# Kernel tuning notes

Measured on AMD Instinct MI355X. Metric: run time of the kernel, lower is better.

The kernel has to match this reference:

```python
import jax, jax.numpy as jnp
import numpy as np
from jax import lax

EPS = 1e-5

def gelu(x):
    return jax.nn.gelu(x, approximate=False)  # torch nn.GELU default (erf)

def conv1d(x, w, b):
    # x: (N, Cin, L), w: (Cout, Cin, K), SAME padding, stride 1
    y = lax.conv_general_dilated(x, w, window_strides=(1,), padding='SAME',
                                 dimension_numbers=('NCH', 'OIH', 'NCH'))
    return y + b[None, :, None]

def setup_inputs() -> dict:
    key = jax.random.key(0)
    ks = jax.random.split(key, 16)
    B, C, P, L, D = 8, 129, 62, 20, 256
    s = lambda k, shape, fan: jax.random.normal(k, shape, jnp.float32) * (1.0 / np.sqrt(fan))
    return {
        'x': jax.random.normal(ks[0], (B, C, P, L), jnp.float32),
        'conv1_w': s(ks[1], (64, 1, 3), 3),   'conv1_b': jnp.zeros((64,), jnp.float32),
        'conv2_w': s(ks[2], (128, 64, 3), 192), 'conv2_b': jnp.zeros((128,), jnp.float32),
        'conv3_w': s(ks[3], (D, 128, 3), 384),  'conv3_b': jnp.zeros((D,), jnp.float32),
        'mix_w': s(ks[4], (C, C), C), 'mix_b': jnp.zeros((C,), jnp.float32),
        'ln_w': jnp.ones((C,), jnp.float32), 'ln_b': jnp.zeros((C,), jnp.float32),
        'proj_w': s(ks[5], (D, D), D), 'proj_b': jnp.zeros((D,), jnp.float32),
    }

def reference(x, conv1_w, conv1_b, conv2_w, conv2_b, conv3_w, conv3_b,
              mix_w, mix_b, ln_w, ln_b, proj_w, proj_b):
    B, C, P, L = x.shape
    D = conv3_w.shape[0]
    # temporal conv stack over flattened (B*C*P, 1, L)
    h = x.reshape(B * C * P, 1, L)
    h = gelu(conv1d(h, conv1_w, conv1_b))
    h = gelu(conv1d(h, conv2_w, conv2_b))
    N, Ch, Lh = h.shape
    h = h.reshape(N, Ch, Lh // 2, 2).max(axis=-1)  # MaxPool1d(2)
    h = gelu(conv1d(h, conv3_w, conv3_b))
    feat = h.mean(axis=-1)                                  # (B*C*P, D)
    feat = feat.reshape(B, C, P, D).transpose(0, 2, 1, 3)   # (B, P, C, D)
    t = feat.reshape(B * P, C, D).transpose(0, 2, 1)        # (B*P, D, C) == per-feature slices
    # channel_mix: Linear(C,C) + GELU + LayerNorm(C), vectorized over the dim axis
    m = gelu(jnp.einsum('ndc,oc->ndo', t, mix_w) + mix_b)
    mu = m.mean(axis=-1, keepdims=True)
    var = ((m - mu) ** 2).mean(axis=-1, keepdims=True)
    m = (m - mu) * lax.rsqrt(var + EPS) * ln_w + ln_b
    mixed = m.transpose(0, 2, 1).reshape(B, P, C, D)
    out = jnp.einsum('bpcd,ed->bpce', mixed, proj_w) + proj_b
    return out.transpose(0, 2, 1, 3)                        # (B, C, P, D)
```

## Files before the change

### kernel.cpp

```cpp
#include <hip/hip_runtime.h>

#define B_ 8
#define C_ 129
#define P_ 62
#define L_ 20
#define D_ 256
#define NSEG (B_*C_*P_)
#define N2   (B_*P_)
#define SEGB 8
#define NWG  (NSEG/SEGB)

#define S1 1416
#define S2 1544

#define FT_STRIDE 168
#define MT_STRIDE 264

typedef short short8 __attribute__((ext_vector_type(8)));
typedef float f32x4  __attribute__((ext_vector_type(4)));

__device__ __forceinline__ float gelu_f(float x) {
    float u   = 0.70710678f * x;
    float au  = __builtin_fabsf(u);
    float den = fmaf(0.47047f, au, 1.0f);
    float t   = __builtin_amdgcn_rcpf(den);
    float q   = fmaf(0.7478556f, t, -0.0958798f);
    q = fmaf(q, t, 0.3480242f);
    float P  = q * t;
    float z  = (-1.4426950409f * au) * au;
    float e  = __builtin_amdgcn_exp2f(z);
    float ea = fmaf(-P, e, 1.0f);
    float er = copysignf(ea, x);
    float hx = 0.5f * x;
    return fmaf(hx, er, hx);
}
__device__ __forceinline__ unsigned short f2bf(float f) {
    unsigned u = __float_as_uint(f);
    u = u + 0x7FFFu + ((u >> 16) & 1u);
    return (unsigned short)(u >> 16);
}
__device__ __forceinline__ unsigned cvt_pk_bf16(float lo, float hi) {
    unsigned r;
    asm("v_cvt_pk_bf16_f32 %0, %1, %2" : "=v"(r) : "v"(lo), "v"(hi));
    return r;
}

__global__ void prep_kernel(const float* __restrict__ w2, const float* __restrict__ w3,
                            const float* __restrict__ mw, const float* __restrict__ pw,
                            const float* __restrict__ mixb, const float* __restrict__ lnw,
                            const float* __restrict__ lnb,
                            unsigned short* __restrict__ A2p, unsigned short* __restrict__ A3p,
                            unsigned short* __restrict__ mixA, unsigned short* __restrict__ projA,
                            float* __restrict__ bmixp, float* __restrict__ lnwp,
                            float* __restrict__ lnbp) {
    int idx = blockIdx.x * blockDim.x + threadIdx.x;
    int stride = gridDim.x * blockDim.x;
    for (int f = idx; f < 6*8*64*8; f += stride) {
        int j = f & 7, ln = (f >> 3) & 63, mt = (f >> 9) & 7, kt = f >> 12;
        int co = mt*16 + (ln & 15);
        int k  = kt >> 1;
        int ci = (kt & 1)*32 + (ln >> 4)*8 + j;
        A2p[f] = f2bf(w2[(co*64 + ci)*3 + k]);
    }
    for (int f = idx; f < 12*16*64*8; f += stride) {
        int j = f & 7, ln = (f >> 3) & 63, mt = (f >> 9) & 15, kt = f >> 13;
        int co = mt*16 + (ln & 15);
        int k  = kt >> 2;
        int ci = (kt & 3)*32 + (ln >> 4)*8 + j;
        A3p[f] = f2bf(w3[(co*128 + ci)*3 + k]);
    }
    for (int f = idx; f < 5*9*64*8; f += stride) {
        int j = f & 7, ln = (f >> 3) & 63;
        int mt = (f >> 9) % 9, kt = (f >> 9) / 9;
        int o = mt*16 + (ln & 15);
        int c = kt*32 + (ln >> 4)*8 + j;
        mixA[f] = (o < 129 && c < 129) ? f2bf(mw[o*129 + c]) : (unsigned short)0;
    }
    for (int f = idx; f < 8*16*64*8; f += stride) {
        int j = f & 7, ln = (f >> 3) & 63, mt = (f >> 9) & 15, kt = f >> 13;
        int e = mt*16 + (ln & 15);
        int d = kt*32 + (ln >> 4)*8 + j;
        projA[f] = f2bf(pw[e*256 + d]);
    }
    for (int i = idx; i < 144; i += stride) {
        bmixp[i] = (i < 129) ? mixb[i] : 0.f;
        lnwp[i]  = (i < 129) ? lnw[i]  : 0.f;
        lnbp[i]  = (i < 129) ? lnb[i]  : 0.f;
    }
}

__global__ __launch_bounds__(512, 2) void conv_mfma_kernel(
    const float* __restrict__ x,
    const float* __restrict__ w1, const float* __restrict__ b1,
    const unsigned short* __restrict__ A2p, const float* __restrict__ b2,
    const unsigned short* __restrict__ A3p, const float* __restrict__ b3,
    unsigned short* __restrict__ feat)
{
    __shared__ __align__(16) unsigned short h1T[SEGB * S1];
    __shared__ __align__(16) unsigned short hpT[SEGB * S2];
    __shared__ float xs[SEGB][22];

    const int t = threadIdx.x;
    const int wave = t >> 6, lane = t & 63;
    const int sL = lane & 15, gL = lane >> 4;
    const int seg8 = sL & 7, hi8 = sL >> 3;
    const int seg0 = blockIdx.x * SEGB;

    for (int idx = t; idx < SEGB*22; idx += 512) {
        int s = idx / 22, i = idx % 22;
        float v = 0.f;
        if (i >= 1 && i <= 20) v = x[(seg0 + s)*L_ + i - 1];
        xs[s][i] = v;
    }
    for (int idx = t; idx < SEGB*64; idx += 512) {
        int s = idx >> 6, ci = idx & 63;
        h1T[s*S1 + ci] = 0;
        h1T[s*S1 + 21*64 + ci] = 0;
    }
    for (int idx = t; idx < SEGB*128; idx += 512) {
        int s = idx >> 7, co = idx & 127;
        hpT[s*S2 + co] = 0;
        hpT[s*S2 + 11*128 + co] = 0;
    }
    __syncthreads();

    {
        int seg = wave;
        int cp = (lane >> 1) & 31, ph = lane & 1;
        int ci0 = cp * 2;
        float wa0 = w1[ci0*3+0], wa1 = w1[ci0*3+1], wa2 = w1[ci0*3+2], ba = b1[ci0];
        float wb0 = w1[ci0*3+3], wb1 = w1[ci0*3+4], wb2 = w1[ci0*3+5], bb = b1[ci0+1];
        unsigned short* dst = &h1T[seg*S1 + ci0];
        #pragma unroll
        for (int i = 0; i < 10; ++i) {
            int l = ph*10 + i;
            float x0 = xs[seg][l], x1 = xs[seg][l+1], x2v = xs[seg][l+2];
            float va = fmaf(x0, wa0, fmaf(x1, wa1, fmaf(x2v, wa2, ba)));
            float vb = fmaf(x0, wb0, fmaf(x1, wb1, fmaf(x2v, wb2, bb)));
            *(unsigned*)(dst + (l+1)*64) = cvt_pk_bf16(gelu_f(va), gelu_f(vb));
        }
    }
    __syncthreads();

    {
        const int mh = wave & 3, ng = wave >> 2;
        f32x4 bias[2];
        #pragma unroll
        for (int mi = 0; mi < 2; ++mi) {
            float4 bb = *(const float4*)(b2 + (mh*2 + mi)*16 + gL*4);
            bias[mi] = (f32x4){bb.x, bb.y, bb.z, bb.w};
        }
        f32x4 acc[2][5];
        #pragma unroll
        for (int mi = 0; mi < 2; ++mi)
            #pragma unroll
            for (int n = 0; n < 5; ++n) acc[mi][n] = bias[mi];

        const unsigned short* h1base = &h1T[seg8*S1 + (ng*10 + hi8)*64 + gL*8];
        #pragma unroll
        for (int h = 0; h < 2; ++h) {
            short8 br[11];
            #pragma unroll
            for (int r = 0; r < 11; ++r)
                br[r] = *(const short8*)(h1base + r*64 + h*32);
            #pragma unroll
            for (int k = 0; k < 3; ++k) {
                int kt = k*2 + h;
                short8 a0 = *(const short8*)(A2p + (((kt*8 + mh*2 + 0)*64 + lane) << 3));
                short8 a1 = *(const short8*)(A2p + (((kt*8 + mh*2 + 1)*64 + lane) << 3));
                #pragma unroll
                for (int n = 0; n < 5; ++n) {
                    acc[0][n] = __builtin_amdgcn_mfma_f32_16x16x32_bf16(a0, br[2*n+k], acc[0][n], 0, 0, 0);
                    acc[1][n] = __builtin_amdgcn_mfma_f32_16x16x32_bf16(a1, br[2*n+k], acc[1][n], 0, 0, 0);
                }
            }
        }
        #pragma unroll
        for (int mi = 0; mi < 2; ++mi) {
            int mt = mh*2 + mi;
            int co0 = mt*16 + gL*4;
            #pragma unroll
            for (int n = 0; n < 5; ++n) {
                int lp = ng*5 + n;
                float pv[4];
                #pragma unroll
                for (int r = 0; r < 4; ++r) {
                    float g = gelu_f(acc[mi][n][r]);
                    pv[r] = fmaxf(g, __shfl_xor(g, 8));
                }
                if (hi8 == 0) {
                    uint2 pk;
                    pk.x = cvt_pk_bf16(pv[0], pv[1]);
                    pk.y = cvt_pk_bf16(pv[2], pv[3]);
                    *(uint2*)&hpT[seg8*S2 + (lp+1)*128 + co0] = pk;
                }
            }
        }
    }
    __syncthreads();

    {
        f32x4 bias[2];
        #pragma unroll
        for (int mi = 0; mi < 2; ++mi) {
            float4 bv = *(const float4*)(b3 + (wave*2 + mi)*16 + gL*4);
            bias[mi] = (f32x4){bv.x, bv.y, bv.z, bv.w};
        }
        f32x4 acc[2][5];
        #pragma unroll
        for (int mi = 0; mi < 2; ++mi)
            #pragma unroll
            for (int n = 0; n < 5; ++n) acc[mi][n] = bias[mi];

        const unsigned short* hpbase = &hpT[seg8*S2 + hi8*128 + gL*8];
        #pragma unroll
        for (int q = 0; q < 4; ++q) {
            short8 br[11];
            #pragma unroll
            for (int r = 0; r < 11; ++r)
                br[r] = *(const short8*)(hpbase + r*128 + q*32);
            #pragma unroll
            for (int k = 0; k < 3; ++k) {
                int kt = k*4 + q;
                short8 a0 = *(const short8*)(A3p + (((kt*16 + wave*2 + 0)*64 + lane) << 3));
                short8 a1 = *(const short8*)(A3p + (((kt*16 + wave*2 + 1)*64 + lane) << 3));
                #pragma unroll
                for (int n = 0; n < 5; ++n) {
                    acc[0][n] = __builtin_amdgcn_mfma_f32_16x16x32_bf16(a0, br[2*n+k], acc[0][n], 0, 0, 0);
                    acc[1][n] = __builtin_amdgcn_mfma_f32_16x16x32_bf16(a1, br[2*n+k], acc[1][n], 0, 0, 0);
                }
            }
        }
        int seg = seg0 + seg8;
        int bI = seg / (C_*P_);
        int rem = seg % (C_*P_);
        int c = rem / P_, p = rem % P_;
        unsigned short* frow = feat + (((size_t)(bI*P_ + p)*C_ + c) << 8);
        #pragma unroll
        for (int mi = 0; mi < 2; ++mi) {
            int co0 = (wave*2 + mi)*16 + gL*4;
            float sum[4] = {0.f, 0.f, 0.f, 0.f};
            #pragma unroll
            for (int n = 0; n < 5; ++n)
                #pragma unroll
                for (int r = 0; r < 4; ++r)
                    sum[r] += gelu_f(acc[mi][n][r]);
            #pragma unroll
            for (int r = 0; r < 4; ++r)
                sum[r] += __shfl_xor(sum[r], 8);
            if (hi8 == 0) {
                uint2 o;
                o.x = cvt_pk_bf16(sum[0]*0.1f, sum[1]*0.1f);
                o.y = cvt_pk_bf16(sum[2]*0.1f, sum[3]*0.1f);
                *(uint2*)(frow + co0) = o;
            }
        }
    }
}

__global__ __launch_bounds__(512, 2) void mix_proj_kernel(
    const unsigned short* __restrict__ feat,
    const unsigned short* __restrict__ mixA, const float* __restrict__ bmixp,
    const float* __restrict__ lnwp, const float* __restrict__ lnbp,
    const unsigned short* __restrict__ projA, const float* __restrict__ proj_b,
    float* __restrict__ out)
{
    __shared__ __align__(16) unsigned short ulds[256*FT_STRIDE];
    unsigned short* fT = ulds;
    unsigned short* mT = ulds;

    const int t = threadIdx.x;
    const int wave = t >> 6, lane = t & 63;
    const int sL = lane & 15, gL = lane >> 4;
    const int n2 = blockIdx.x;
    const int b = n2 / P_, p = n2 % P_;

    const unsigned* fbase32 = (const unsigned*)(feat + (size_t)n2 * C_ * 256);
    for (int idx = t; idx < 129*128; idx += 512) {
        int c = idx >> 7, q = idx & 127;
        unsigned v = fbase32[idx];
        int d0 = q * 2;
        fT[d0*FT_STRIDE + c]     = (unsigned short)(v & 0xFFFFu);
        fT[(d0+1)*FT_STRIDE + c] = (unsigned short)(v >> 16);
    }
    for (int idx = t; idx < 256*31; idx += 512) {
        int d = idx / 31, c = 129 + idx % 31;
        fT[d*FT_STRIDE + c] = 0;
    }
    __syncthreads();

    f32x4 acc[9][2];
    #pragma unroll
    for (int mt = 0; mt < 9; ++mt) {
        float4 bv = *(const float4*)(bmixp + mt*16 + gL*4);
        f32x4 bi = (f32x4){bv.x, bv.y, bv.z, bv.w};
        acc[mt][0] = bi;
        acc[mt][1] = bi;
    }

    #pragma unroll
    for (int kt = 0; kt < 5; ++kt) {
        short8 bb[2];
        #pragma unroll
        for (int nt = 0; nt < 2; ++nt) {
            int d = (wave*2 + nt)*16 + sL;
            bb[nt] = *(const short8*)&fT[d*FT_STRIDE + kt*32 + gL*8];
        }
        #pragma unroll
        for (int mt = 0; mt < 9; ++mt) {
            short8 a = *(const short8*)(mixA + (((kt*9 + mt)*64 + lane) << 3));
            #pragma unroll
            for (int nt = 0; nt < 2; ++nt)
                acc[mt][nt] = __builtin_amdgcn_mfma_f32_16x16x32_bf16(a, bb[nt], acc[mt][nt], 0, 0, 0);
        }
    }

    float sum[2] = {0.f, 0.f}, sq[2] = {0.f, 0.f};
    #pragma unroll
    for (int mt = 0; mt < 9; ++mt) {
        #pragma unroll
        for (int nt = 0; nt < 2; ++nt) {
            #pragma unroll
            for (int r = 0; r < 4; ++r) {
                float g = gelu_f(acc[mt][nt][r]);
                acc[mt][nt][r] = g;
                sum[nt] += g;
                sq[nt]  += g*g;
            }
        }
    }
    float mu[2], rs[2];
    #pragma unroll
    for (int nt = 0; nt < 2; ++nt) {
        float s = sum[nt], q = sq[nt];
        s += __shfl_xor(s, 16); q += __shfl_xor(q, 16);
        s += __shfl_xor(s, 32); q += __shfl_xor(q, 32);
        mu[nt] = s * (1.f/129.f);
        float var = q * (1.f/129.f) - mu[nt]*mu[nt];
        rs[nt] = rsqrtf(var + 1e-5f);
    }

    __syncthreads();

    #pragma unroll
    for (int mt = 0; mt < 9; ++mt) {
        float4 lw = *(const float4*)(lnwp + mt*16 + gL*4);
        float4 lb = *(const float4*)(lnbp + mt*16 + gL*4);
        float lwr[4] = {lw.x, lw.y, lw.z, lw.w};
        float lbr[4] = {lb.x, lb.y, lb.z, lb.w};
        #pragma unroll
        for (int nt = 0; nt < 2; ++nt) {
            int d = (wave*2 + nt)*16 + sL;
            #pragma unroll
            for (int r = 0; r < 4; ++r) {
                int o = mt*16 + gL*4 + r;
                float y = (acc[mt][nt][r] - mu[nt]) * rs[nt] * lwr[r] + lbr[r];
                mT[o*MT_STRIDE + d] = f2bf(y);
            }
        }
    }
    __syncthreads();

    f32x4 pacc[2][9];
    #pragma unroll
    for (int mi = 0; mi < 2; ++mi)
        #pragma unroll
        for (int nt = 0; nt < 9; ++nt) pacc[mi][nt] = (f32x4){0.f,0.f,0.f,0.f};

    #pragma unroll
    for (int kt = 0; kt < 8; ++kt) {
        short8 a[2];
        #pragma unroll
        for (int mi = 0; mi < 2; ++mi)
            a[mi] = *(const short8*)(projA + (((kt*16 + wave*2 + mi)*64 + lane) << 3));
        #pragma unroll
        for (int nt = 0; nt < 9; ++nt) {
            short8 bb = *(const short8*)&mT[(nt*16 + sL)*MT_STRIDE + kt*32 + gL*8];
            #pragma unroll
            for (int mi = 0; mi < 2; ++mi)
                pacc[mi][nt] = __builtin_amdgcn_mfma_f32_16x16x32_bf16(a[mi], bb, pacc[mi][nt], 0, 0, 0);
        }
    }

    #pragma unroll
    for (int mi = 0; mi < 2; ++mi) {
        int e0 = (wave*2 + mi)*16 + gL*4;
        float4 pb4 = *(const float4*)(proj_b + e0);
        #pragma unroll
        for (int nt = 0; nt < 9; ++nt) {
            int c = nt*16 + sL;
            if (c < 129) {
                float4 o4;
                o4.x = pacc[mi][nt][0] + pb4.x;
                o4.y = pacc[mi][nt][1] + pb4.y;
                o4.z = pacc[mi][nt][2] + pb4.z;
                o4.w = pacc[mi][nt][3] + pb4.w;
                *(float4*)&out[(((size_t)(b*C_ + c)*P_) + p)*256 + e0] = o4;
            }
        }
    }
}

extern "C" void kernel_launch(void* const* d_in, const int* in_sizes, int n_in,
                              void* d_out, int out_size, void* d_ws, size_t ws_size,
                              hipStream_t stream) {
    (void)in_sizes; (void)n_in; (void)out_size; (void)ws_size;
    const float* x    = (const float*)d_in[0];
    const float* w1   = (const float*)d_in[1];
    const float* b1   = (const float*)d_in[2];
    const float* w2   = (const float*)d_in[3];
    const float* b2   = (const float*)d_in[4];
    const float* w3   = (const float*)d_in[5];
    const float* b3   = (const float*)d_in[6];
    const float* mixw = (const float*)d_in[7];
    const float* mixb = (const float*)d_in[8];
    const float* lnw  = (const float*)d_in[9];
    const float* lnb  = (const float*)d_in[10];
    const float* pw   = (const float*)d_in[11];
    const float* pb   = (const float*)d_in[12];
    float* out = (float*)d_out;
    float* ws  = (float*)d_ws;

    unsigned short* feat = (unsigned short*)ws;
    unsigned short* A2p  = (unsigned short*)(ws + 16379904);
    unsigned short* A3p  = A2p + 24576;
    unsigned short* mixA = A3p + 98304;
    unsigned short* projA = mixA + 23040;
    float* bmixp = (float*)(projA + 65536);
    float* lnwp  = bmixp + 144;
    float* lnbp  = lnwp + 144;

    prep_kernel<<<256, 256, 0, stream>>>(w2, w3, mixw, pw, mixb, lnw, lnb,
                                         A2p, A3p, mixA, projA, bmixp, lnwp, lnbp);
    conv_mfma_kernel<<<NWG, 512, 0, stream>>>(x, w1, b1, A2p, b2, A3p, b3, feat);
    mix_proj_kernel<<<N2, 512, 0, stream>>>(feat, mixA, bmixp, lnwp, lnbp, projA, pb, out);
}
```

Baseline: 352.3 us.

## Restructure conv MFMA tiling to 4 segments per block with 4 positions per tile

New measurement: 420.6 us. 1.19x slower.

```diff
diff --git a/kernel.cpp b/kernel.cpp
--- a/kernel.cpp
+++ b/kernel.cpp
@@ -7,11 +7,11 @@
 #define D_ 256
 #define NSEG (B_*C_*P_)
 #define N2   (B_*P_)
-#define SEGB 8
+#define SEGB 4
 #define NWG  (NSEG/SEGB)
 
-#define S1 1416
-#define S2 1544
+#define S1 1424
+#define S2 1808
 
 #define FT_STRIDE 168
 #define MT_STRIDE 264
@@ -89,7 +89,7 @@
     }
 }
 
-__global__ __launch_bounds__(512, 2) void conv_mfma_kernel(
+__global__ __launch_bounds__(512, 4) void conv_mfma_kernel(
     const float* __restrict__ x,
     const float* __restrict__ w1, const float* __restrict__ b1,
     const unsigned short* __restrict__ A2p, const float* __restrict__ b2,
@@ -103,37 +103,40 @@
     const int t = threadIdx.x;
     const int wave = t >> 6, lane = t & 63;
     const int sL = lane & 15, gL = lane >> 4;
-    const int seg8 = sL & 7, hi8 = sL >> 3;
+    const int seg4 = sL & 3, p0 = sL >> 2;
     const int seg0 = blockIdx.x * SEGB;
 
-    for (int idx = t; idx < SEGB*22; idx += 512) {
-        int s = idx / 22, i = idx % 22;
+    if (t < SEGB*22) {
+        int s = t / 22, i = t % 22;
         float v = 0.f;
         if (i >= 1 && i <= 20) v = x[(seg0 + s)*L_ + i - 1];
         xs[s][i] = v;
     }
-    for (int idx = t; idx < SEGB*64; idx += 512) {
-        int s = idx >> 6, ci = idx & 63;
+    if (t < SEGB*64) {
+        int s = t >> 6, ci = t & 63;
         h1T[s*S1 + ci] = 0;
         h1T[s*S1 + 21*64 + ci] = 0;
     }
-    for (int idx = t; idx < SEGB*128; idx += 512) {
-        int s = idx >> 7, co = idx & 127;
-        hpT[s*S2 + co] = 0;
-        hpT[s*S2 + 11*128 + co] = 0;
+    for (int idx = t; idx < SEGB*4*128; idx += 512) {
+        int s = idx >> 9;
+        int r2 = (idx >> 7) & 3;
+        int row = (r2 == 0) ? 0 : 10 + r2;
+        int co = idx & 127;
+        hpT[s*S2 + row*128 + co] = 0;
     }
     __syncthreads();
 
     {
-        int seg = wave;
-        int cp = (lane >> 1) & 31, ph = lane & 1;
+        int seg = wave & 3, phh = wave >> 2;
+        int cp = lane & 31, pq = lane >> 5;
         int ci0 = cp * 2;
+        int l0 = phh*10 + pq*5;
         float wa0 = w1[ci0*3+0], wa1 = w1[ci0*3+1], wa2 = w1[ci0*3+2], ba = b1[ci0];
         float wb0 = w1[ci0*3+3], wb1 = w1[ci0*3+4], wb2 = w1[ci0*3+5], bb = b1[ci0+1];
         unsigned short* dst = &h1T[seg*S1 + ci0];
         #pragma unroll
-        for (int i = 0; i < 10; ++i) {
-            int l = ph*10 + i;
+        for (int i = 0; i < 5; ++i) {
+            int l = l0 + i;
             float x0 = xs[seg][l], x1 = xs[seg][l+1], x2v = xs[seg][l+2];
             float va = fmaf(x0, wa0, fmaf(x1, wa1, fmaf(x2v, wa2, ba)));
             float vb = fmaf(x0, wb0, fmaf(x1, wb1, fmaf(x2v, wb2, bb)));
@@ -143,112 +146,105 @@
     __syncthreads();
 
     {
-        const int mh = wave & 3, ng = wave >> 2;
-        f32x4 bias[2];
-        #pragma unroll
-        for (int mi = 0; mi < 2; ++mi) {
-            float4 bb = *(const float4*)(b2 + (mh*2 + mi)*16 + gL*4);
-            bias[mi] = (f32x4){bb.x, bb.y, bb.z, bb.w};
-        }
-        f32x4 acc[2][5];
-        #pragma unroll
-        for (int mi = 0; mi < 2; ++mi)
-            #pragma unroll
-            for (int n = 0; n < 5; ++n) acc[mi][n] = bias[mi];
-
-        const unsigned short* h1base = &h1T[seg8*S1 + (ng*10 + hi8)*64 + gL*8];
+        f32x4 acc[5];
+        {
+            float4 bb = *(const float4*)(b2 + wave*16 + gL*4);
+            f32x4 bi = (f32x4){bb.x, bb.y, bb.z, bb.w};
+            #pragma unroll
+            for (int n = 0; n < 5; ++n) acc[n] = bi;
+        }
+        const unsigned short* h1b = &h1T[seg4*S1 + p0*64 + gL*8];
         #pragma unroll
         for (int h = 0; h < 2; ++h) {
-            short8 br[11];
-            #pragma unroll
-            for (int r = 0; r < 11; ++r)
-                br[r] = *(const short8*)(h1base + r*64 + h*32);
-            #pragma unroll
-            for (int k = 0; k < 3; ++k) {
-                int kt = k*2 + h;
-                short8 a0 = *(const short8*)(A2p + (((kt*8 + mh*2 + 0)*64 + lane) << 3));
-                short8 a1 = *(const short8*)(A2p + (((kt*8 + mh*2 + 1)*64 + lane) << 3));
-                #pragma unroll
-                for (int n = 0; n < 5; ++n) {
-                    acc[0][n] = __builtin_amdgcn_mfma_f32_16x16x32_bf16(a0, br[2*n+k], acc[0][n], 0, 0, 0);
-                    acc[1][n] = __builtin_amdgcn_mfma_f32_16x16x32_bf16(a1, br[2*n+k], acc[1][n], 0, 0, 0);
-                }
-            }
-        }
-        #pragma unroll
-        for (int mi = 0; mi < 2; ++mi) {
-            int mt = mh*2 + mi;
-            int co0 = mt*16 + gL*4;
-            #pragma unroll
-            for (int n = 0; n < 5; ++n) {
-                int lp = ng*5 + n;
-                float pv[4];
-                #pragma unroll
-                for (int r = 0; r < 4; ++r) {
-                    float g = gelu_f(acc[mi][n][r]);
-                    pv[r] = fmaxf(g, __shfl_xor(g, 8));
-                }
-                if (hi8 == 0) {
-                    uint2 pk;
-                    pk.x = cvt_pk_bf16(pv[0], pv[1]);
-                    pk.y = cvt_pk_bf16(pv[2], pv[3]);
-                    *(uint2*)&hpT[seg8*S2 + (lp+1)*128 + co0] = pk;
-                }
+            short8 a0 = *(const short8*)(A2p + ((((0*2+h)*8 + wave)*64 + lane) << 3));
+            short8 a1 = *(const short8*)(A2p + ((((1*2+h)*8 + wave)*64 + lane) << 3));
+            short8 a2 = *(const short8*)(A2p + ((((2*2+h)*8 + wave)*64 + lane) << 3));
+            #pragma unroll
+            for (int tt = 0; tt < 5; ++tt) {
+                const unsigned short* rb = h1b + (4*tt)*64 + h*32;
+                short8 b0 = *(const short8*)(rb);
+                short8 b1 = *(const short8*)(rb + 64);
+                short8 b2v = *(const short8*)(rb + 128);
+                acc[tt] = __builtin_amdgcn_mfma_f32_16x16x32_bf16(a0, b0, acc[tt], 0, 0, 0);
+                acc[tt] = __builtin_amdgcn_mfma_f32_16x16x32_bf16(a1, b1, acc[tt], 0, 0, 0);
+                acc[tt] = __builtin_amdgcn_mfma_f32_16x16x32_bf16(a2, b2v, acc[tt], 0, 0, 0);
+            }
+        }
+        int co0 = wave*16 + gL*4;
+        #pragma unroll
+        for (int tt = 0; tt < 5; ++tt) {
+            float pv[4];
+            #pragma unroll
+            for (int r = 0; r < 4; ++r) {
+                float g = gelu_f(acc[tt][r]);
+                pv[r] = fmaxf(g, __shfl_xor(g, 4));
+            }
+            if ((p0 & 1) == 0) {
+                int lp = 2*tt + (p0 >> 1);
+                uint2 pk;
+                pk.x = cvt_pk_bf16(pv[0], pv[1]);
+                pk.y = cvt_pk_bf16(pv[2], pv[3]);
+                *(uint2*)&hpT[seg4*S2 + (lp+1)*128 + co0] = pk;
             }
         }
     }
     __syncthreads();
 
     {
-        f32x4 bias[2];
+        f32x4 acc[2][3];
         #pragma unroll
         for (int mi = 0; mi < 2; ++mi) {
             float4 bv = *(const float4*)(b3 + (wave*2 + mi)*16 + gL*4);
-            bias[mi] = (f32x4){bv.x, bv.y, bv.z, bv.w};
-        }
-        f32x4 acc[2][5];
-        #pragma unroll
-        for (int mi = 0; mi < 2; ++mi)
-            #pragma unroll
-            for (int n = 0; n < 5; ++n) acc[mi][n] = bias[mi];
-
-        const unsigned short* hpbase = &hpT[seg8*S2 + hi8*128 + gL*8];
+            f32x4 bi = (f32x4){bv.x, bv.y, bv.z, bv.w};
+            #pragma unroll
+            for (int n = 0; n < 3; ++n) acc[mi][n] = bi;
+        }
+        const unsigned short* hpb = &hpT[seg4*S2 + p0*128 + gL*8];
         #pragma unroll
         for (int q = 0; q < 4; ++q) {
-            short8 br[11];
-            #pragma unroll
-            for (int r = 0; r < 11; ++r)
-                br[r] = *(const short8*)(hpbase + r*128 + q*32);
-            #pragma unroll
-            for (int k = 0; k < 3; ++k) {
-                int kt = k*4 + q;
-                short8 a0 = *(const short8*)(A3p + (((kt*16 + wave*2 + 0)*64 + lane) << 3));
-                short8 a1 = *(const short8*)(A3p + (((kt*16 + wave*2 + 1)*64 + lane) << 3));
+            short8 a[3][2];
+            #pragma unroll
+            for (int k = 0; k < 3; ++k)
                 #pragma unroll
-                for (int n = 0; n < 5; ++n) {
-                    acc[0][n] = __builtin_amdgcn_mfma_f32_16x16x32_bf16(a0, br[2*n+k], acc[0][n], 0, 0, 0);
-                    acc[1][n] = __builtin_amdgcn_mfma_f32_16x16x32_bf16(a1, br[2*n+k], acc[1][n], 0, 0, 0);
+                for (int mi = 0; mi < 2; ++mi)
+                    a[k][mi] = *(const short8*)(A3p + ((((k*4+q)*16 + wave*2 + mi)*64 + lane) << 3));
+            #pragma unroll
+            for (int tt = 0; tt < 3; ++tt) {
+                const unsigned short* rb = hpb + (4*tt)*128 + q*32;
+                short8 b0 = *(const short8*)(rb);
+                short8 b1 = *(const short8*)(rb + 128);
+                short8 b2v = *(const short8*)(rb + 256);
+                #pragma unroll
+                for (int mi = 0; mi < 2; ++mi) {
+                    acc[mi][tt] = __builtin_amdgcn_mfma_f32_16x16x32_bf16(a[0][mi], b0, acc[mi][tt], 0, 0, 0);
+                    acc[mi][tt] = __builtin_amdgcn_mfma_f32_16x16x32_bf16(a[1][mi], b1, acc[mi][tt], 0, 0, 0);
+                    acc[mi][tt] = __builtin_amdgcn_mfma_f32_16x16x32_bf16(a[2][mi], b2v, acc[mi][tt], 0, 0, 0);
                 }
             }
         }
-        int seg = seg0 + seg8;
+        int seg = seg0 + seg4;
         int bI = seg / (C_*P_);
         int rem = seg % (C_*P_);
         int c = rem / P_, p = rem % P_;
         unsigned short* frow = feat + (((size_t)(bI*P_ + p)*C_ + c) << 8);
+        float msk2 = (p0 < 2) ? 1.f : 0.f;
         #pragma unroll
         for (int mi = 0; mi < 2; ++mi) {
-            int co0 = (wave*2 + mi)*16 + gL*4;
             float sum[4] = {0.f, 0.f, 0.f, 0.f};
             #pragma unroll
-            for (int n = 0; n < 5; ++n)
+            for (int tt = 0; tt < 3; ++tt) {
+                float m = (tt == 2) ? msk2 : 1.f;
                 #pragma unroll
                 for (int r = 0; r < 4; ++r)
-                    sum[r] += gelu_f(acc[mi][n][r]);
-            #pragma unroll
-            for (int r = 0; r < 4; ++r)
+                    sum[r] = fmaf(gelu_f(acc[mi][tt][r]), m, sum[r]);
+            }
+            #pragma unroll
+            for (int r = 0; r < 4; ++r) {
+                sum[r] += __shfl_xor(sum[r], 4);
                 sum[r] += __shfl_xor(sum[r], 8);
-            if (hi8 == 0) {
+            }
+            if (p0 == 0) {
+                int co0 = (wave*2 + mi)*16 + gL*4;
                 uint2 o;
                 o.x = cvt_pk_bf16(sum[0]*0.1f, sum[1]*0.1f);
                 o.y = cvt_pk_bf16(sum[2]*0.1f, sum[3]*0.1f);
```
